# Kernel optimization log

Hardware: AMD Instinct MI355X
Metric: run time of the kernel (lower is better)

## Reference

```python
import jax, jax.numpy as jnp
import numpy as np

EPS = 1e-5

def _bn(x, g, b, m, v):
    # inference-mode batchnorm with moving statistics
    return (x - m) * jax.lax.rsqrt(v + EPS) * g + b

def setup_inputs() -> dict:
    key = jax.random.key(0)
    ks = jax.random.split(key, 12)
    t, b, s, hu = 512, 64, 1024, 1024
    d_in = s + hu
    si = jax.random.normal(ks[0], (b, s), dtype=jnp.float32)
    h = jax.random.normal(ks[1], (t, b, hu), dtype=jnp.float32)
    W0 = jax.random.normal(ks[2], (d_in, 10), dtype=jnp.float32) * 0.02
    b0 = jnp.zeros((10,), jnp.float32)
    g0 = jnp.ones((10,), jnp.float32)
    be0 = jnp.zeros((10,), jnp.float32)
    m0 = jax.random.normal(ks[3], (10,), dtype=jnp.float32) * 0.1
    v0 = jax.random.uniform(ks[4], (10,), dtype=jnp.float32) + 0.5
    W1 = jax.random.normal(ks[5], (10, 5), dtype=jnp.float32) * 0.3
    b1 = jnp.zeros((5,), jnp.float32)
    g1 = jnp.ones((5,), jnp.float32)
    be1 = jnp.zeros((5,), jnp.float32)
    m1 = jax.random.normal(ks[6], (5,), dtype=jnp.float32) * 0.1
    v1 = jax.random.uniform(ks[7], (5,), dtype=jnp.float32) + 0.5
    W2 = jax.random.normal(ks[8], (5, 1), dtype=jnp.float32) * 0.4
    b2 = jnp.zeros((1,), jnp.float32)
    return {"si": si, "h": h, "W0": W0, "b0": b0, "g0": g0, "be0": be0,
            "m0": m0, "v0": v0, "W1": W1, "b1": b1, "g1": g1, "be1": be1,
            "m1": m1, "v1": v1, "W2": W2, "b2": b2}

def reference(si, h, W0, b0, g0, be0, m0, v0, W1, b1, g1, be1, m1, v1, W2, b2):
    t, b, hu = h.shape
    # concat decoder state with every encoder hidden state: [t, b, s+hu]
    x = jnp.concatenate([jnp.broadcast_to(si[None], (t,) + si.shape), h], axis=-1)
    x = jax.nn.relu(_bn(x @ W0 + b0, g0, be0, m0, v0))
    x = jax.nn.relu(_bn(x @ W1 + b1, g1, be1, m1, v1))
    scores = x @ W2 + b2                       # [t, b, 1]
    # original: tf.concat over axis 0 -> [t*b, 1], softmax over axis 0 (ALL t*b entries)
    a = jax.nn.softmax(scores.reshape(t * b))  # [t*b]
    # original uses only the first t rows of the flattened softmax as scalar weights
    ci = jnp.einsum('t,tbh->bh', a[:t], h)     # [b, hu]
    return ci
```

## Files before the change

kernel.cpp:

```cpp
#include <hip/hip_runtime.h>

#define EPS 1e-5f

constexpr int T  = 512;
constexpr int B  = 64;
constexpr int HU = 1024;
constexpr int S  = 1024;
constexpr int C  = B * HU;
constexpr int TSPLIT = 32;

constexpr size_t OFF_SIW0 = 0;
constexpr size_t OFF_W    = 1024;
constexpr size_t OFF_ESC  = 2048;
constexpr size_t OFF_PART = 35840;

__device__ __forceinline__ float mlp_head(
    const float* __restrict__ u10,
    const float* __restrict__ b0, const float* __restrict__ g0,
    const float* __restrict__ be0,const float* __restrict__ m0,
    const float* __restrict__ v0,
    const float* __restrict__ W1, const float* __restrict__ b1,
    const float* __restrict__ g1, const float* __restrict__ be1,
    const float* __restrict__ m1, const float* __restrict__ v1,
    const float* __restrict__ W2, const float* __restrict__ b2) {
    float y[10];
#pragma unroll
    for (int j = 0; j < 10; ++j) {
        float u = (u10[j] + b0[j] - m0[j]) * (1.0f / sqrtf(v0[j] + EPS)) * g0[j]
                  + be0[j];
        y[j] = fmaxf(u, 0.f);
    }
    float z[5];
#pragma unroll
    for (int i = 0; i < 5; ++i) {
        float u = b1[i];
#pragma unroll
        for (int j = 0; j < 10; ++j) u = fmaf(y[j], W1[j * 5 + i], u);
        u = (u - m1[i]) * (1.0f / sqrtf(v1[i] + EPS)) * g1[i] + be1[i];
        z[i] = fmaxf(u, 0.f);
    }
    float sc = b2[0];
#pragma unroll
    for (int i = 0; i < 5; ++i) sc = fmaf(z[i], W2[i], sc);
    return sc;
}

__global__ __launch_bounds__(256) void k_weights(
    const float* __restrict__ h,  const float* __restrict__ si,
    const float* __restrict__ W0,
    const float* __restrict__ b0, const float* __restrict__ g0,
    const float* __restrict__ be0,const float* __restrict__ m0,
    const float* __restrict__ v0,
    const float* __restrict__ W1, const float* __restrict__ b1,
    const float* __restrict__ g1, const float* __restrict__ be1,
    const float* __restrict__ m1, const float* __restrict__ v1,
    const float* __restrict__ W2, const float* __restrict__ b2,
    float* __restrict__ w, float* __restrict__ siW0out) {
    const int e   = blockIdx.x;
    const int t   = e >> 6;
    const int cb  = e & 63;
    const int tid = threadIdx.x;
    const int wv  = tid >> 6, ln = tid & 63;

    const float4 hv = *(const float4*)(h  + (size_t)t  * C + (size_t)cb * HU + tid * 4);
    const float4 sv = *(const float4*)(si + (size_t)cb * S + tid * 4);
    const float* wsb = W0 + (size_t)(4 * tid) * 10;
    const float* whb = W0 + (size_t)(1024 + 4 * tid) * 10;

    float ssi[10], shh[10];
#pragma unroll
    for (int j = 0; j < 10; ++j) { ssi[j] = 0.f; shh[j] = 0.f; }
#pragma unroll
    for (int d = 0; d < 4; ++d) {
        const float sx = (&sv.x)[d], hx = (&hv.x)[d];
#pragma unroll
        for (int j = 0; j < 10; ++j) {
            ssi[j] = fmaf(sx, wsb[d * 10 + j], ssi[j]);
            shh[j] = fmaf(hx, whb[d * 10 + j], shh[j]);
        }
    }
#pragma unroll
    for (int j = 0; j < 10; ++j) {
#pragma unroll
        for (int off = 32; off > 0; off >>= 1) {
            ssi[j] += __shfl_down(ssi[j], off, 64);
            shh[j] += __shfl_down(shh[j], off, 64);
        }
    }
    __shared__ float rs[4][10], rh[4][10];
    if (ln == 0) {
#pragma unroll
        for (int j = 0; j < 10; ++j) { rs[wv][j] = ssi[j]; rh[wv][j] = shh[j]; }
    }
    __syncthreads();

    if (t == 0 && tid < 10)
        siW0out[cb * 10 + tid] = rs[0][tid] + rs[1][tid] + rs[2][tid] + rs[3][tid];

    if (tid == 0) {
        float u10[10];
#pragma unroll
        for (int j = 0; j < 10; ++j)
            u10[j] = rs[0][j] + rs[1][j] + rs[2][j] + rs[3][j] +
                     rh[0][j] + rh[1][j] + rh[2][j] + rh[3][j];
        const float sc = mlp_head(u10, b0, g0, be0, m0, v0,
                                  W1, b1, g1, be1, m1, v1, W2, b2);
        w[t * 64 + cb] = expf(sc);
    }
}

__global__ __launch_bounds__(256) void k_fused(
    const float* __restrict__ h,  const float* __restrict__ W0,
    const float* __restrict__ w,  const float* __restrict__ siW0,
    const float* __restrict__ b0, const float* __restrict__ g0,
    const float* __restrict__ be0,const float* __restrict__ m0,
    const float* __restrict__ v0,
    const float* __restrict__ W1, const float* __restrict__ b1,
    const float* __restrict__ g1, const float* __restrict__ be1,
    const float* __restrict__ m1, const float* __restrict__ v1,
    const float* __restrict__ W2, const float* __restrict__ b2,
    float* __restrict__ escore, float* __restrict__ part) {
    const int cb  = blockIdx.x & 63;
    const int ts  = blockIdx.x >> 6;
    const int tid = threadIdx.x;
    const int wv  = tid >> 6, ln = tid & 63;

    float wf[40];
    {
        const float4* wb = (const float4*)(W0 + (size_t)(1024 + 4 * tid) * 10);
#pragma unroll
        for (int q = 0; q < 10; ++q) {
            const float4 v4 = wb[q];
            wf[4 * q + 0] = v4.x; wf[4 * q + 1] = v4.y;
            wf[4 * q + 2] = v4.z; wf[4 * q + 3] = v4.w;
        }
    }

    __shared__ float red[4][16][10];

    const float* hp = h + (size_t)(ts * 16) * C + (size_t)cb * HU + tid * 4;
    const float* wt = w + ts * 16;

    float4 wacc = {0.f, 0.f, 0.f, 0.f};
    float4 hv = *(const float4*)(hp);

#pragma unroll 4
    for (int i = 0; i < 16; ++i) {
        const float4 hcur = hv;
        if (i + 1 < 16)
            hv = *(const float4*)(hp + (size_t)(i + 1) * C);

        const float av = wt[i];
        wacc.x = fmaf(av, hcur.x, wacc.x);
        wacc.y = fmaf(av, hcur.y, wacc.y);
        wacc.z = fmaf(av, hcur.z, wacc.z);
        wacc.w = fmaf(av, hcur.w, wacc.w);

        float sacc[10];
#pragma unroll
        for (int j = 0; j < 10; ++j) sacc[j] = 0.f;
#pragma unroll
        for (int d = 0; d < 4; ++d) {
            const float hx = (&hcur.x)[d];
#pragma unroll
            for (int j = 0; j < 10; ++j)
                sacc[j] = fmaf(hx, wf[d * 10 + j], sacc[j]);
        }
#pragma unroll
        for (int j = 0; j < 10; ++j) {
#pragma unroll
            for (int off = 32; off > 0; off >>= 1)
                sacc[j] += __shfl_down(sacc[j], off, 64);
        }
        if (ln == 0) {
#pragma unroll
            for (int j = 0; j < 10; ++j) red[wv][i][j] = sacc[j];
        }
    }

    *(float4*)(part + (size_t)ts * C + (size_t)cb * HU + tid * 4) = wacc;

    __syncthreads();
    if (tid < 16) {
        float u10[10];
#pragma unroll
        for (int j = 0; j < 10; ++j)
            u10[j] = red[0][tid][j] + red[1][tid][j] + red[2][tid][j] +
                     red[3][tid][j] + siW0[cb * 10 + j];
        const float sc = mlp_head(u10, b0, g0, be0, m0, v0,
                                  W1, b1, g1, be1, m1, v1, W2, b2);
        escore[(ts * 16 + tid) * 64 + cb] = expf(sc);
    }
}

__global__ __launch_bounds__(256) void k_out(const float* __restrict__ part,
                                             const float* __restrict__ escore,
                                             float* __restrict__ out) {
    const int tid = threadIdx.x;
    const int wv  = tid >> 6, ln = tid & 63;

    float zs = 0.f;
#pragma unroll
    for (int q = 0; q < 32; ++q) {
        const float4 v = ((const float4*)escore)[tid + 256 * q];
        zs += v.x + v.y + v.z + v.w;
    }
#pragma unroll
    for (int off = 32; off > 0; off >>= 1)
        zs += __shfl_down(zs, off, 64);
    __shared__ float zr[4];
    __shared__ float sinv;
    if (ln == 0) zr[wv] = zs;
    __syncthreads();
    if (tid == 0) sinv = 1.0f / (zr[0] + zr[1] + zr[2] + zr[3]);
    __syncthreads();
    const float invZ = sinv;

    const int c = blockIdx.x * 1024 + tid * 4;
    float4 s = {0.f, 0.f, 0.f, 0.f};
#pragma unroll 8
    for (int ts = 0; ts < TSPLIT; ++ts) {
        const float4 v = *(const float4*)(part + (size_t)ts * C + c);
        s.x += v.x; s.y += v.y; s.z += v.z; s.w += v.w;
    }
    s.x *= invZ; s.y *= invZ; s.z *= invZ; s.w *= invZ;
    *(float4*)(out + c) = s;
}

extern "C" void kernel_launch(void* const* d_in, const int* in_sizes, int n_in,
                              void* d_out, int out_size, void* d_ws, size_t ws_size,
                              hipStream_t stream) {
    const float* si  = (const float*)d_in[0];
    const float* h   = (const float*)d_in[1];
    const float* W0  = (const float*)d_in[2];
    const float* b0  = (const float*)d_in[3];
    const float* g0  = (const float*)d_in[4];
    const float* be0 = (const float*)d_in[5];
    const float* m0  = (const float*)d_in[6];
    const float* v0  = (const float*)d_in[7];
    const float* W1  = (const float*)d_in[8];
    const float* b1  = (const float*)d_in[9];
    const float* g1  = (const float*)d_in[10];
    const float* be1 = (const float*)d_in[11];
    const float* m1  = (const float*)d_in[12];
    const float* v1  = (const float*)d_in[13];
    const float* W2  = (const float*)d_in[14];
    const float* b2  = (const float*)d_in[15];

    float* ws     = (float*)d_ws;
    float* siW0   = ws + OFF_SIW0;
    float* w      = ws + OFF_W;
    float* escore = ws + OFF_ESC;
    float* part   = ws + OFF_PART;
    float* out    = (float*)d_out;

    hipLaunchKernelGGL(k_weights, dim3(512),  dim3(256), 0, stream, h, si, W0,
                       b0, g0, be0, m0, v0, W1, b1, g1, be1, m1, v1, W2, b2,
                       w, siW0);
    hipLaunchKernelGGL(k_fused,   dim3(2048), dim3(256), 0, stream, h, W0, w, siW0,
                       b0, g0, be0, m0, v0, W1, b1, g1, be1, m1, v1, W2, b2,
                       escore, part);
    hipLaunchKernelGGL(k_out,     dim3(64),   dim3(256), 0, stream, part, escore, out);
}
```

Measured before the change: 283.7 us.

## Stage h tiles in LDS to compute scores and weighted sums per block

The fused kernel now has each block own one batch column and a 64-step time chunk. It streams 128-wide K slices of h through a padded shared-memory tile with register double-buffering, so each thread accumulates its own time step's 10-wide projection without per-step cross-lane shuffle reductions. The weighted sum over time is computed from the same tile, which cuts the part buffer from 32 slices to 8 and shortens the k_out reduction. The trade-offs are only 512 blocks (less parallelism for hiding latency), W0 read from global memory inside the inner loop rather than held in registers, and an extra sync per chunk.

```diff
diff --git a/kernel.cpp b/kernel.cpp
--- a/kernel.cpp
+++ b/kernel.cpp
@@ -7,7 +7,11 @@
 constexpr int HU = 1024;
 constexpr int S  = 1024;
 constexpr int C  = B * HU;
-constexpr int TSPLIT = 32;
+constexpr int TCHUNK = 64;
+constexpr int NTC = T / TCHUNK;
+constexpr int KC  = 128;
+constexpr int NCH = HU / KC;
+constexpr int LDR = KC + 1;
 
 constexpr size_t OFF_SIW0 = 0;
 constexpr size_t OFF_W    = 1024;
@@ -109,7 +113,7 @@
     }
 }
 
-__global__ __launch_bounds__(256) void k_fused(
+__global__ __launch_bounds__(256) void k_mega(
     const float* __restrict__ h,  const float* __restrict__ W0,
     const float* __restrict__ w,  const float* __restrict__ siW0,
     const float* __restrict__ b0, const float* __restrict__ g0,
@@ -120,76 +124,83 @@
     const float* __restrict__ m1, const float* __restrict__ v1,
     const float* __restrict__ W2, const float* __restrict__ b2,
     float* __restrict__ escore, float* __restrict__ part) {
-    const int cb  = blockIdx.x & 63;
-    const int ts  = blockIdx.x >> 6;
+    const int b   = blockIdx.x & 63;
+    const int tc  = blockIdx.x >> 6;
     const int tid = threadIdx.x;
     const int wv  = tid >> 6, ln = tid & 63;
 
-    float wf[40];
-    {
-        const float4* wb = (const float4*)(W0 + (size_t)(1024 + 4 * tid) * 10);
-#pragma unroll
-        for (int q = 0; q < 10; ++q) {
-            const float4 v4 = wb[q];
-            wf[4 * q + 0] = v4.x; wf[4 * q + 1] = v4.y;
-            wf[4 * q + 2] = v4.z; wf[4 * q + 3] = v4.w;
-        }
-    }
-
-    __shared__ float red[4][16][10];
-
-    const float* hp = h + (size_t)(ts * 16) * C + (size_t)cb * HU + tid * 4;
-    const float* wt = w + ts * 16;
-
-    float4 wacc = {0.f, 0.f, 0.f, 0.f};
-    float4 hv = *(const float4*)(hp);
-
-#pragma unroll 4
-    for (int i = 0; i < 16; ++i) {
-        const float4 hcur = hv;
-        if (i + 1 < 16)
-            hv = *(const float4*)(hp + (size_t)(i + 1) * C);
-
-        const float av = wt[i];
-        wacc.x = fmaf(av, hcur.x, wacc.x);
-        wacc.y = fmaf(av, hcur.y, wacc.y);
-        wacc.z = fmaf(av, hcur.z, wacc.z);
-        wacc.w = fmaf(av, hcur.w, wacc.w);
-
-        float sacc[10];
-#pragma unroll
-        for (int j = 0; j < 10; ++j) sacc[j] = 0.f;
-#pragma unroll
-        for (int d = 0; d < 4; ++d) {
-            const float hx = (&hcur.x)[d];
+    __shared__ float sh[64 * LDR];
+    __shared__ float park[4][64][10];
+    __shared__ float wsl[64];
+
+    if (tid < 64) wsl[tid] = w[tc * 64 + tid];
+
+    const float* hb = h + (size_t)(tc * 64) * C + (size_t)b * HU;
+    const int srow = tid >> 5;
+    const int scol = (tid & 31) * 4;
+
+    float4 stg[8];
+#pragma unroll
+    for (int q = 0; q < 8; ++q)
+        stg[q] = *(const float4*)(hb + (size_t)(8 * q + srow) * C + scol);
+
+    const int klo = __builtin_amdgcn_readfirstlane(32 * wv);
+    const int kk  = tid >> 1;
+    const int hlf = tid & 1;
+
+    float sacc[10];
+#pragma unroll
+    for (int j = 0; j < 10; ++j) sacc[j] = 0.f;
+
+    for (int c = 0; c < NCH; ++c) {
+        if (c > 0) __syncthreads();
+#pragma unroll
+        for (int q = 0; q < 8; ++q) {
+            float* dst = sh + (8 * q + srow) * LDR + scol;
+            dst[0] = stg[q].x; dst[1] = stg[q].y;
+            dst[2] = stg[q].z; dst[3] = stg[q].w;
+        }
+        if (c + 1 < NCH) {
+#pragma unroll
+            for (int q = 0; q < 8; ++q)
+                stg[q] = *(const float4*)(hb + (size_t)(8 * q + srow) * C +
+                                          (c + 1) * KC + scol);
+        }
+        __syncthreads();
+
+        const float* wp  = W0 + (size_t)(1024 + c * KC + klo) * 10;
+        const float* shp = sh + ln * LDR + klo;
+#pragma unroll
+        for (int i = 0; i < 32; ++i) {
+            const float hx = shp[i];
 #pragma unroll
             for (int j = 0; j < 10; ++j)
-                sacc[j] = fmaf(hx, wf[d * 10 + j], sacc[j]);
-        }
-#pragma unroll
-        for (int j = 0; j < 10; ++j) {
-#pragma unroll
-            for (int off = 32; off > 0; off >>= 1)
-                sacc[j] += __shfl_down(sacc[j], off, 64);
-        }
-        if (ln == 0) {
-#pragma unroll
-            for (int j = 0; j < 10; ++j) red[wv][i][j] = sacc[j];
-        }
-    }
-
-    *(float4*)(part + (size_t)ts * C + (size_t)cb * HU + tid * 4) = wacc;
-
-    __syncthreads();
-    if (tid < 16) {
+                sacc[j] = fmaf(hx, wp[i * 10 + j], sacc[j]);
+        }
+
+        float s = 0.f;
+        const float* shc = sh + (32 * hlf) * LDR + kk;
+        const float* wl  = wsl + 32 * hlf;
+#pragma unroll
+        for (int r = 0; r < 32; ++r)
+            s = fmaf(wl[r], shc[(size_t)r * LDR], s);
+        s += __shfl_xor(s, 1, 64);
+        if (!hlf)
+            part[(size_t)tc * C + (size_t)b * HU + c * KC + kk] = s;
+    }
+
+#pragma unroll
+    for (int j = 0; j < 10; ++j) park[wv][ln][j] = sacc[j];
+    __syncthreads();
+    if (tid < 64) {
         float u10[10];
 #pragma unroll
         for (int j = 0; j < 10; ++j)
-            u10[j] = red[0][tid][j] + red[1][tid][j] + red[2][tid][j] +
-                     red[3][tid][j] + siW0[cb * 10 + j];
+            u10[j] = park[0][tid][j] + park[1][tid][j] + park[2][tid][j] +
+                     park[3][tid][j] + siW0[b * 10 + j];
         const float sc = mlp_head(u10, b0, g0, be0, m0, v0,
                                   W1, b1, g1, be1, m1, v1, W2, b2);
-        escore[(ts * 16 + tid) * 64 + cb] = expf(sc);
+        escore[(size_t)(tc * 64 + tid) * 64 + b] = expf(sc);
     }
 }
 
@@ -218,8 +229,8 @@
 
     const int c = blockIdx.x * 1024 + tid * 4;
     float4 s = {0.f, 0.f, 0.f, 0.f};
-#pragma unroll 8
-    for (int ts = 0; ts < TSPLIT; ++ts) {
+#pragma unroll
+    for (int ts = 0; ts < NTC; ++ts) {
         const float4 v = *(const float4*)(part + (size_t)ts * C + c);
         s.x += v.x; s.y += v.y; s.z += v.z; s.w += v.w;
     }
@@ -254,11 +265,11 @@
     float* part   = ws + OFF_PART;
     float* out    = (float*)d_out;
 
-    hipLaunchKernelGGL(k_weights, dim3(512),  dim3(256), 0, stream, h, si, W0,
+    hipLaunchKernelGGL(k_weights, dim3(512), dim3(256), 0, stream, h, si, W0,
                        b0, g0, be0, m0, v0, W1, b1, g1, be1, m1, v1, W2, b2,
                        w, siW0);
-    hipLaunchKernelGGL(k_fused,   dim3(2048), dim3(256), 0, stream, h, W0, w, siW0,
+    hipLaunchKernelGGL(k_mega,    dim3(512), dim3(256), 0, stream, h, W0, w, siW0,
                        b0, g0, be0, m0, v0, W1, b1, g1, be1, m1, v1, W2, b2,
                        escore, part);
-    hipLaunchKernelGGL(k_out,     dim3(64),   dim3(256), 0, stream, part, escore, out);
-}
+    hipLaunchKernelGGL(k_out,     dim3(64),  dim3(256), 0, stream, part, escore, out);
+}
```

Result: faster. 272.9 us (-3.8%).

## Restructure streaming kernel so each wave owns time steps, with transposed W0

Applied to the files above, without the earlier changes.

Replaces the block-per-16-timesteps fused kernel with one where each wave handles 8 time steps for one batch row, in two passes of 4. Each loaded W0 column is reused across 4 rows, and the cross-lane reductions drop from one per timestep to one batch per group of four, with no shared memory or block barrier. A small transpose kernel lays out W0 so lane-contiguous loads work. This adds a launch, doubles the partial slabs that k_out must reduce, and uses scalar rather than float4 loads of h.

```diff
diff --git a/kernel.cpp b/kernel.cpp
--- a/kernel.cpp
+++ b/kernel.cpp
@@ -7,12 +7,13 @@
 constexpr int HU = 1024;
 constexpr int S  = 1024;
 constexpr int C  = B * HU;
-constexpr int TSPLIT = 32;
+constexpr int NSLAB = 64;
 
 constexpr size_t OFF_SIW0 = 0;
 constexpr size_t OFF_W    = 1024;
 constexpr size_t OFF_ESC  = 2048;
-constexpr size_t OFF_PART = 35840;
+constexpr size_t OFF_W0T  = 34816;
+constexpr size_t OFF_PART = 45056;
 
 __device__ __forceinline__ float mlp_head(
     const float* __restrict__ u10,
@@ -43,6 +44,20 @@
 #pragma unroll
     for (int i = 0; i < 5; ++i) sc = fmaf(z[i], W2[i], sc);
     return sc;
+}
+
+__global__ __launch_bounds__(1024) void k_tr(const float* __restrict__ W0,
+                                             float* __restrict__ W0T) {
+    const int k = threadIdx.x;
+    const float* src = W0 + (size_t)(1024 + k) * 10;
+    float v[10];
+#pragma unroll
+    for (int q = 0; q < 5; ++q) {
+        const float2 p = ((const float2*)src)[q];
+        v[2 * q] = p.x; v[2 * q + 1] = p.y;
+    }
+#pragma unroll
+    for (int j = 0; j < 10; ++j) W0T[j * 1024 + k] = v[j];
 }
 
 __global__ __launch_bounds__(256) void k_weights(
@@ -109,8 +124,8 @@
     }
 }
 
-__global__ __launch_bounds__(256) void k_fused(
-    const float* __restrict__ h,  const float* __restrict__ W0,
+__global__ __launch_bounds__(256, 4) void k_stream(
+    const float* __restrict__ h,  const float* __restrict__ W0T,
     const float* __restrict__ w,  const float* __restrict__ siW0,
     const float* __restrict__ b0, const float* __restrict__ g0,
     const float* __restrict__ be0,const float* __restrict__ m0,
@@ -120,77 +135,75 @@
     const float* __restrict__ m1, const float* __restrict__ v1,
     const float* __restrict__ W2, const float* __restrict__ b2,
     float* __restrict__ escore, float* __restrict__ part) {
-    const int cb  = blockIdx.x & 63;
-    const int ts  = blockIdx.x >> 6;
-    const int tid = threadIdx.x;
-    const int wv  = tid >> 6, ln = tid & 63;
-
-    float wf[40];
-    {
-        const float4* wb = (const float4*)(W0 + (size_t)(1024 + 4 * tid) * 10);
-#pragma unroll
-        for (int q = 0; q < 10; ++q) {
-            const float4 v4 = wb[q];
-            wf[4 * q + 0] = v4.x; wf[4 * q + 1] = v4.y;
-            wf[4 * q + 2] = v4.z; wf[4 * q + 3] = v4.w;
-        }
-    }
-
-    __shared__ float red[4][16][10];
-
-    const float* hp = h + (size_t)(ts * 16) * C + (size_t)cb * HU + tid * 4;
-    const float* wt = w + ts * 16;
-
-    float4 wacc = {0.f, 0.f, 0.f, 0.f};
-    float4 hv = *(const float4*)(hp);
+    const int b    = blockIdx.x & 63;
+    const int tg   = blockIdx.x >> 6;
+    const int wv   = threadIdx.x >> 6;
+    const int ln   = threadIdx.x & 63;
+    const int t0   = tg * 32 + wv * 8;
+    const int slab = tg * 4 + wv;
+
+    float acc[16];
+#pragma unroll
+    for (int s = 0; s < 16; ++s) acc[s] = 0.f;
+
+#pragma unroll
+    for (int pass = 0; pass < 2; ++pass) {
+        const int tA = t0 + pass * 4;
+        const float* hp = h + ((size_t)tA * 64 + b) * HU;
+        const float wt0 = w[tA + 0], wt1 = w[tA + 1];
+        const float wt2 = w[tA + 2], wt3 = w[tA + 3];
+
+        float sacc[4][10];
+#pragma unroll
+        for (int r = 0; r < 4; ++r)
+#pragma unroll
+            for (int j = 0; j < 10; ++j) sacc[r][j] = 0.f;
 
 #pragma unroll 4
-    for (int i = 0; i < 16; ++i) {
-        const float4 hcur = hv;
-        if (i + 1 < 16)
-            hv = *(const float4*)(hp + (size_t)(i + 1) * C);
-
-        const float av = wt[i];
-        wacc.x = fmaf(av, hcur.x, wacc.x);
-        wacc.y = fmaf(av, hcur.y, wacc.y);
-        wacc.z = fmaf(av, hcur.z, wacc.z);
-        wacc.w = fmaf(av, hcur.w, wacc.w);
-
-        float sacc[10];
-#pragma unroll
-        for (int j = 0; j < 10; ++j) sacc[j] = 0.f;
-#pragma unroll
-        for (int d = 0; d < 4; ++d) {
-            const float hx = (&hcur.x)[d];
-#pragma unroll
-            for (int j = 0; j < 10; ++j)
-                sacc[j] = fmaf(hx, wf[d * 10 + j], sacc[j]);
-        }
-#pragma unroll
-        for (int j = 0; j < 10; ++j) {
-#pragma unroll
-            for (int off = 32; off > 0; off >>= 1)
-                sacc[j] += __shfl_down(sacc[j], off, 64);
-        }
-        if (ln == 0) {
-#pragma unroll
-            for (int j = 0; j < 10; ++j) red[wv][i][j] = sacc[j];
-        }
-    }
-
-    *(float4*)(part + (size_t)ts * C + (size_t)cb * HU + tid * 4) = wacc;
-
-    __syncthreads();
-    if (tid < 16) {
-        float u10[10];
-#pragma unroll
-        for (int j = 0; j < 10; ++j)
-            u10[j] = red[0][tid][j] + red[1][tid][j] + red[2][tid][j] +
-                     red[3][tid][j] + siW0[cb * 10 + j];
-        const float sc = mlp_head(u10, b0, g0, be0, m0, v0,
-                                  W1, b1, g1, be1, m1, v1, W2, b2);
-        escore[(ts * 16 + tid) * 64 + cb] = expf(sc);
-    }
+        for (int s = 0; s < 16; ++s) {
+            const int k = 64 * s + ln;
+            float w0t[10];
+#pragma unroll
+            for (int j = 0; j < 10; ++j) w0t[j] = W0T[j * 1024 + k];
+
+            const float hx0 = hp[k];
+            const float hx1 = hp[(size_t)1 * 64 * HU + k];
+            const float hx2 = hp[(size_t)2 * 64 * HU + k];
+            const float hx3 = hp[(size_t)3 * 64 * HU + k];
+#pragma unroll
+            for (int j = 0; j < 10; ++j) {
+                sacc[0][j] = fmaf(hx0, w0t[j], sacc[0][j]);
+                sacc[1][j] = fmaf(hx1, w0t[j], sacc[1][j]);
+                sacc[2][j] = fmaf(hx2, w0t[j], sacc[2][j]);
+                sacc[3][j] = fmaf(hx3, w0t[j], sacc[3][j]);
+            }
+            acc[s] = fmaf(wt0, hx0, acc[s]);
+            acc[s] = fmaf(wt1, hx1, acc[s]);
+            acc[s] = fmaf(wt2, hx2, acc[s]);
+            acc[s] = fmaf(wt3, hx3, acc[s]);
+        }
+
+#pragma unroll
+        for (int r = 0; r < 4; ++r) {
+            float u10[10];
+#pragma unroll
+            for (int j = 0; j < 10; ++j) {
+                float v = sacc[r][j];
+#pragma unroll
+                for (int off = 32; off > 0; off >>= 1)
+                    v += __shfl_xor(v, off, 64);
+                u10[j] = v + siW0[b * 10 + j];
+            }
+            const float sc = mlp_head(u10, b0, g0, be0, m0, v0,
+                                      W1, b1, g1, be1, m1, v1, W2, b2);
+            if (ln == 0)
+                escore[(size_t)(tA + r) * 64 + b] = expf(sc);
+        }
+    }
+
+    float* pp = part + (size_t)slab * C + (size_t)b * HU;
+#pragma unroll
+    for (int s = 0; s < 16; ++s) pp[64 * s + ln] = acc[s];
 }
 
 __global__ __launch_bounds__(256) void k_out(const float* __restrict__ part,
@@ -219,8 +232,8 @@
     const int c = blockIdx.x * 1024 + tid * 4;
     float4 s = {0.f, 0.f, 0.f, 0.f};
 #pragma unroll 8
-    for (int ts = 0; ts < TSPLIT; ++ts) {
-        const float4 v = *(const float4*)(part + (size_t)ts * C + c);
+    for (int sl = 0; sl < NSLAB; ++sl) {
+        const float4 v = *(const float4*)(part + (size_t)sl * C + c);
         s.x += v.x; s.y += v.y; s.z += v.z; s.w += v.w;
     }
     s.x *= invZ; s.y *= invZ; s.z *= invZ; s.w *= invZ;
@@ -251,14 +264,17 @@
     float* siW0   = ws + OFF_SIW0;
     float* w      = ws + OFF_W;
     float* escore = ws + OFF_ESC;
+    float* W0T    = ws + OFF_W0T;
     float* part   = ws + OFF_PART;
     float* out    = (float*)d_out;
 
-    hipLaunchKernelGGL(k_weights, dim3(512),  dim3(256), 0, stream, h, si, W0,
+    hipLaunchKernelGGL(k_tr,      dim3(1),    dim3(1024), 0, stream, W0, W0T);
+    hipLaunchKernelGGL(k_weights, dim3(512),  dim3(256),  0, stream, h, si, W0,
                        b0, g0, be0, m0, v0, W1, b1, g1, be1, m1, v1, W2, b2,
                        w, siW0);
-    hipLaunchKernelGGL(k_fused,   dim3(2048), dim3(256), 0, stream, h, W0, w, siW0,
-                       b0, g0, be0, m0, v0, W1, b1, g1, be1, m1, v1, W2, b2,
-                       escore, part);
-    hipLaunchKernelGGL(k_out,     dim3(64),   dim3(256), 0, stream, part, escore, out);
-}
+    hipLaunchKernelGGL(k_stream,  dim3(1024), dim3(256),  0, stream, h, W0T, w,
+                       siW0, b0, g0, be0, m0, v0, W1, b1, g1, be1, m1, v1,
+                       W2, b2, escore, part);
+    hipLaunchKernelGGL(k_out,     dim3(64),   dim3(256),  0, stream, part,
+                       escore, out);
+}
```

After: 288.4 us. No clear change (+1.6%).
